# Kernel optimization log

Hardware: AMD Instinct MI355X
Metric: run time of the kernel (lower is better)

The kernel has to match this reference:

```python
import jax, jax.numpy as jnp
import numpy as np

S, B, H = 2048, 1, 1024
N_HEADS = 16
HEAD_DIM = H // N_HEADS
E, K, F = 8, 2, 2048  # experts, top_k, ffn_hidden
EPS = 1e-5


def layernorm(x, w, b):
    mu = jnp.mean(x, axis=-1, keepdims=True)
    var = jnp.mean(jnp.square(x - mu), axis=-1, keepdims=True)
    return (x - mu) * jax.lax.rsqrt(var + EPS) * w + b


def setup_inputs() -> dict:
    key = jax.random.key(0)
    ks = jax.random.split(key, 8)
    std = 0.02
    return {
        "x": jax.random.normal(ks[0], (S, B, H), dtype=jnp.float32),
        "ln1_w": jnp.ones((H,), jnp.float32),
        "ln1_b": jnp.zeros((H,), jnp.float32),
        "in_proj_w": jax.random.normal(ks[1], (3 * H, H), jnp.float32) * std,
        "in_proj_b": jnp.zeros((3 * H,), jnp.float32),
        "out_proj_w": jax.random.normal(ks[2], (H, H), jnp.float32) * std,
        "out_proj_b": jnp.zeros((H,), jnp.float32),
        "ln2_w": jnp.ones((H,), jnp.float32),
        "ln2_b": jnp.zeros((H,), jnp.float32),
        "router_w": jax.random.normal(ks[3], (E, H), jnp.float32) * std,
        "w1": jax.random.normal(ks[4], (E, H, F), jnp.float32) * std,
        "w2": jax.random.normal(ks[5], (E, F, H), jnp.float32) * std,
    }


def reference(x, ln1_w, ln1_b, in_proj_w, in_proj_b, out_proj_w, out_proj_b,
              ln2_w, ln2_b, router_w, w1, w2):
    s, b, h = x.shape
    # ---- causal self-attention (nn.MultiheadAttention math) ----
    hn = layernorm(x, ln1_w, ln1_b)
    qkv = hn @ in_proj_w.T + in_proj_b          # [S,B,3H]
    q, k, v = jnp.split(qkv, 3, axis=-1)
    q = q.reshape(s, b, N_HEADS, HEAD_DIM)
    k = k.reshape(s, b, N_HEADS, HEAD_DIM)
    v = v.reshape(s, b, N_HEADS, HEAD_DIM)
    scores = jnp.einsum('sbnd,tbnd->bnst', q, k) / np.sqrt(HEAD_DIM)
    causal = jnp.tril(jnp.ones((s, s), bool))
    scores = jnp.where(causal[None, None], scores, -jnp.inf)
    probs = jax.nn.softmax(scores, axis=-1)
    attn = jnp.einsum('bnst,tbnd->sbnd', probs, v).reshape(s, b, h)
    attn = attn @ out_proj_w.T + out_proj_b
    x1 = x + attn
    # ---- dMoE FFN: router softmax -> top-k gates -> expert GELU MLP ----
    hn2 = layernorm(x1, ln2_w, ln2_b).reshape(s * b, h)   # tokens [T,H]
    logits = hn2 @ router_w.T                              # [T,E]
    rp = jax.nn.softmax(logits, axis=-1)
    topw, topi = jax.lax.top_k(rp, K)                      # [T,K]
    gates = jnp.sum(jax.nn.one_hot(topi, E, dtype=hn2.dtype) * topw[..., None], axis=1)  # [T,E]
    hmid = jax.nn.gelu(jnp.einsum('th,ehf->tef', hn2, w1), approximate=False)  # [T,E,F]
    y = jnp.einsum('tef,efh->th', hmid * gates[:, :, None], w2)                # [T,H]
    return x1 + y.reshape(s, b, h)
```

## Files before the change

### kernel.cpp

```cpp
#include <hip/hip_runtime.h>

#define SL 2048
#define HID 1024
#define NHEAD 16
#define HD 64
#define NEXP 8
#define FF 2048
#define MAXTILE 40
#define MAXROWS (MAXTILE * 128)
#define CPAD 32

typedef short bf16x8 __attribute__((ext_vector_type(8)));
typedef float f32x4 __attribute__((ext_vector_type(4)));
typedef unsigned u32x4 __attribute__((ext_vector_type(4)));

__device__ __forceinline__ unsigned short f2bf(float f) {
  unsigned u = __builtin_bit_cast(unsigned, f);
  u += 0x7fffu + ((u >> 16) & 1u);
  return (unsigned short)(u >> 16);
}

__device__ __forceinline__ void gload16(const void* g, void* l) {
  __builtin_amdgcn_global_load_lds((const __attribute__((address_space(1))) void*)g,
                                   (__attribute__((address_space(3))) void*)l,
                                   16, 0, 0);
}

__device__ __forceinline__ void xcd_remap(int& bx, int& by) {
  const int nx = gridDim.x;
  const int nwg = nx * gridDim.y;
  const int L = by * nx + bx;
  const int per = nwg >> 3;
  const int Lp = (L & 7) * per + (L >> 3);
  bx = Lp % nx;
  by = Lp / nx;
}

struct TransLds { float Afp[64 * 128]; unsigned Bu[128 * 33]; };

__device__ __forceinline__ void trans_tile(
    int tile, const float* __restrict__ w1, const float* __restrict__ w2,
    unsigned short* __restrict__ w1t, unsigned short* __restrict__ w2t,
    int tid, TransLds* T)
{
  const int m = tile >> 8;
  const int t = tile & 255;
  const float* in;
  unsigned short* out;
  int R, C, r0, c0;
  if (m < 8) {
    in = w1 + (size_t)m * HID * FF;  out = w1t + (size_t)m * HID * FF;
    R = HID; C = FF;  r0 = (t >> 4) * 64;  c0 = (t & 15) * 128;
  } else {
    in = w2 + (size_t)(m - 8) * FF * HID;  out = w2t + (size_t)(m - 8) * FF * HID;
    R = FF; C = HID;  r0 = (t >> 3) * 64;  c0 = (t & 7) * 128;
  }
  const int wv = tid >> 6, ln = tid & 63;
#pragma unroll
  for (int p = 0; p < 8; p++) {
    const int ebase = p * 1024 + wv * 256;
    const int eo = ebase + ln * 4;
    const int r = eo >> 7, c = eo & 127;
    gload16(in + (size_t)(r0 + r) * C + c0 + c, (char*)T->Afp + (size_t)ebase * 4);
  }
  asm volatile("s_waitcnt vmcnt(0)" ::: "memory");
  __syncthreads();
#pragma unroll
  for (int it = 0; it < 16; it++) {
    const int idx = it * 256 + tid;
    const int rp = idx >> 7;
    const int c = idx & 127;
    const float v0 = T->Afp[(2 * rp) * 128 + c];
    const float v1 = T->Afp[(2 * rp + 1) * 128 + c];
    T->Bu[c * 33 + rp] = (unsigned)f2bf(v0) | ((unsigned)f2bf(v1) << 16);
  }
  __syncthreads();
#pragma unroll
  for (int it = 0; it < 8; it++) {
    const int idx = it * 256 + tid;
    const int c = idx >> 4;
    const int r4 = (idx & 15) * 4;
    const unsigned u0 = T->Bu[c * 33 + (r4 >> 1)];
    const unsigned u1 = T->Bu[c * 33 + (r4 >> 1) + 1];
    ushort4 u;
    u.x = (unsigned short)(u0 & 0xffff);
    u.y = (unsigned short)(u0 >> 16);
    u.z = (unsigned short)(u1 & 0xffff);
    u.w = (unsigned short)(u1 >> 16);
    *reinterpret_cast<ushort4*>(&out[(size_t)(c0 + c) * R + r0 + r4]) = u;
  }
}

#define PIPE_WAIT(i, NT)                                                     \
  if ((i) == (NT) - 1)                                                       \
    asm volatile("s_waitcnt vmcnt(0) lgkmcnt(0)" ::: "memory");              \
  else                                                                       \
    asm volatile("s_waitcnt vmcnt(4) lgkmcnt(0)" ::: "memory");              \
  __builtin_amdgcn_s_barrier();

#define GEMM_FRAGS_MFMA(CC)                                                  \
  bf16x8 af[4], bfr[4];                                                      \
  _Pragma("unroll")                                                          \
  for (int mt = 0; mt < 4; mt++)                                             \
    af[mt] = *reinterpret_cast<const bf16x8*>(                               \
        &Asm[CC][(wm + mt * 16 + la) * 32 + lk]);                            \
  _Pragma("unroll")                                                          \
  for (int nt = 0; nt < 4; nt++)                                             \
    bfr[nt] = *reinterpret_cast<const bf16x8*>(                              \
        &Bsm[CC][(wn + nt * 16 + la) * 32 + lk]);                            \
  __builtin_amdgcn_s_setprio(1);                                             \
  _Pragma("unroll")                                                          \
  for (int mt = 0; mt < 4; mt++)                                             \
    _Pragma("unroll")                                                        \
    for (int nt = 0; nt < 4; nt++)                                           \
      acc[mt][nt] =                                                          \
          __builtin_amdgcn_mfma_f32_16x16x32_bf16(af[mt], bfr[nt], acc[mt][nt], 0, 0, 0); \
  __builtin_amdgcn_s_setprio(0);

#define PIPE_ROT()                                                           \
  cc = (cc == 2) ? 0 : cc + 1;                                               \
  cs = (cs == 2) ? 0 : cs + 1;

__global__ __launch_bounds__(256) void qkv_trans_kernel(
    const unsigned short* __restrict__ A, const unsigned short* __restrict__ Bt,
    const float* __restrict__ bias,
    unsigned short* __restrict__ q_out, unsigned short* __restrict__ k_out,
    unsigned short* __restrict__ vt_out,
    const float* __restrict__ w1, const float* __restrict__ w2,
    unsigned short* __restrict__ w1t, unsigned short* __restrict__ w2t)
{
  __shared__ union {
    struct { unsigned short A[3][4096]; unsigned short B[3][4096]; } g;
    TransLds t;
  } sm;
  const int tid = threadIdx.x;

  if (blockIdx.z == 0) {
    unsigned short (*Asm)[4096] = sm.g.A;
    unsigned short (*Bsm)[4096] = sm.g.B;
    int bx = blockIdx.x, by = blockIdx.y;
    xcd_remap(bx, by);
    const int wave = tid >> 6;
    const int lane = tid & 63;
    const int m0 = by * 128;
    const int n0 = bx * 128;
    const int wm = (wave >> 1) * 64;
    const int wn = (wave & 1) * 64;
    const int la = lane & 15;
    const int lk = (lane >> 4) * 8;

    f32x4 acc[4][4] = {};

    const int srow = tid >> 2;
    const int skoff = (tid & 3) * 8;
    const unsigned short* Ag = A + (size_t)(m0 + srow) * HID + skoff;
    const unsigned short* Bg = Bt + (size_t)(n0 + srow) * HID + skoff;

    auto stage = [&](int s, int k0) {
      gload16(Ag + k0, &Asm[s][wave * 512]);
      gload16(Ag + (size_t)64 * HID + k0, &Asm[s][2048 + wave * 512]);
      gload16(Bg + k0, &Bsm[s][wave * 512]);
      gload16(Bg + (size_t)64 * HID + k0, &Bsm[s][2048 + wave * 512]);
    };

    stage(0, 0);
    stage(1, 32);
    const int NT = HID >> 5;
    int cc = 0, cs = 2;
    for (int i = 0; i < NT; ++i) {
      PIPE_WAIT(i, NT)
      if (i + 2 < NT) stage(cs, (i + 2) << 5);
      GEMM_FRAGS_MFMA(cc)
      PIPE_ROT()
    }

    const int lg = lane >> 4;
#pragma unroll
    for (int mt = 0; mt < 4; mt++) {
#pragma unroll
      for (int nt = 0; nt < 4; nt++) {
#pragma unroll
        for (int r = 0; r < 4; r++) {
          const int row = m0 + wm + mt * 16 + lg * 4 + r;
          const int col = n0 + wn + nt * 16 + la;
          float v = acc[mt][nt][r] + bias[col];
          const int hh = (col & 1023) >> 6;
          const int dd = col & 63;
          const unsigned short bv = f2bf(v);
          if (col < 1024)
            q_out[(size_t)hh * SL * HD + (size_t)row * HD + dd] = bv;
          else if (col < 2048)
            k_out[(size_t)hh * SL * HD + (size_t)row * HD + dd] = bv;
          else
            vt_out[(size_t)hh * HD * SL + (size_t)dd * SL + row] = bv;
        }
      }
    }
  } else {
    const int id = blockIdx.y * 24 + blockIdx.x;
    const int tile = 512 + ((int)blockIdx.z - 1) * 384 + id;
    trans_tile(tile, w1, w2, w1t, w2t, tid, &sm.t);
  }
}

__global__ __launch_bounds__(256) void gemm_bt2(
    const unsigned short* __restrict__ A, const unsigned short* __restrict__ Bt,
    float* __restrict__ outf,
    const float* __restrict__ w1, const float* __restrict__ w2,
    unsigned short* __restrict__ w1t, unsigned short* __restrict__ w2t)
{
  __shared__ union {
    struct { unsigned short A[3][4096]; unsigned short B[3][4096]; } g;
    TransLds t;
  } sm;
  const int tid = threadIdx.x;

  if (blockIdx.z >= 2) {
    const int id = blockIdx.y * 8 + blockIdx.x;
    const int tile = 3200 + ((int)blockIdx.z - 2) * 128 + id;
    trans_tile(tile, w1, w2, w1t, w2t, tid, &sm.t);
    return;
  }

  unsigned short (*Asm)[4096] = sm.g.A;
  unsigned short (*Bsm)[4096] = sm.g.B;
  int bx = blockIdx.x, by = blockIdx.y;
  xcd_remap(bx, by);
  const int wave = tid >> 6;
  const int lane = tid & 63;
  const int m0 = by * 128;
  const int n0 = bx * 128;
  const int koff = blockIdx.z * (HID / 2);
  const int wm = (wave >> 1) * 64;
  const int wn = (wave & 1) * 64;
  const int la = lane & 15;
  const int lk = (lane >> 4) * 8;

  f32x4 acc[4][4] = {};

  const int srow = tid >> 2;
  const int skoff = (tid & 3) * 8;
  const unsigned short* Ag = A + (size_t)(m0 + srow) * HID + koff + skoff;
  const unsigned short* Bg = Bt + (size_t)(n0 + srow) * HID + koff + skoff;

  auto stage = [&](int s, int k0) {
    gload16(Ag + k0, &Asm[s][wave * 512]);
    gload16(Ag + (size_t)64 * HID + k0, &Asm[s][2048 + wave * 512]);
    gload16(Bg + k0, &Bsm[s][wave * 512]);
    gload16(Bg + (size_t)64 * HID + k0, &Bsm[s][2048 + wave * 512]);
  };

  stage(0, 0);
  stage(1, 32);
  const int NT = (HID / 2) >> 5;
  int cc = 0, cs = 2;
  for (int i = 0; i < NT; ++i) {
    PIPE_WAIT(i, NT)
    if (i + 2 < NT) stage(cs, (i + 2) << 5);
    GEMM_FRAGS_MFMA(cc)
    PIPE_ROT()
  }

  const int lg = lane >> 4;
#pragma unroll
  for (int mt = 0; mt < 4; mt++) {
#pragma unroll
    for (int nt = 0; nt < 4; nt++) {
#pragma unroll
      for (int r = 0; r < 4; r++) {
        const int row = m0 + wm + mt * 16 + lg * 4 + r;
        const int col = n0 + wn + nt * 16 + la;
        outf[(size_t)blockIdx.z * SL * HID + (size_t)row * HID + col] = acc[mt][nt][r];
      }
    }
  }
}

__global__ __launch_bounds__(256) void gemm_moe1(
    const unsigned short* __restrict__ A, const unsigned short* __restrict__ w1t,
    const int* __restrict__ perm, const float* __restrict__ gateg,
    const int* __restrict__ texp, const int* __restrict__ trow,
    unsigned short* __restrict__ hmidg)
{
  __shared__ unsigned short Asm[3][128 * 32];
  __shared__ unsigned short Bsm[3][128 * 32];
  int bx = blockIdx.x, by = blockIdx.y;
  xcd_remap(bx, by);
  const int e = texp[by];
  if (e < 0) return;
  const int row0 = trow[by];
  const int tid = threadIdx.x;
  const int wave = tid >> 6;
  const int lane = tid & 63;
  const int n0 = bx * 128;
  const int wm = (wave >> 1) * 64;
  const int wn = (wave & 1) * 64;
  const int la = lane & 15;
  const int lk = (lane >> 4) * 8;
  f32x4 acc[4][4] = {};

  const int srow = tid >> 2;
  const int skoff = (tid & 3) * 8;
  const int p0 = perm[row0 + srow];
  const int p1 = perm[row0 + 64 + srow];
  const unsigned short* Ag0 = A + (size_t)(p0 < 0 ? 0 : (p0 >> 1)) * HID + skoff;
  const unsigned short* Ag1 = A + (size_t)(p1 < 0 ? 0 : (p1 >> 1)) * HID + skoff;
  const unsigned short* Bg = w1t + (size_t)e * HID * FF + (size_t)(n0 + srow) * HID + skoff;

  auto stage = [&](int s, int k0) {
    gload16(Ag0 + k0, &Asm[s][wave * 512]);
    gload16(Ag1 + k0, &Asm[s][2048 + wave * 512]);
    gload16(Bg + k0, &Bsm[s][wave * 512]);
    gload16(Bg + (size_t)64 * HID + k0, &Bsm[s][2048 + wave * 512]);
  };

  stage(0, 0);
  stage(1, 32);
  const int NT = HID >> 5;
  int cc = 0, cs = 2;
  for (int i = 0; i < NT; ++i) {
    PIPE_WAIT(i, NT)
    if (i + 2 < NT) stage(cs, (i + 2) << 5);
    GEMM_FRAGS_MFMA(cc)
    PIPE_ROT()
  }

  const int lg = lane >> 4;
#pragma unroll
  for (int mt = 0; mt < 4; mt++) {
    float gr[4];
#pragma unroll
    for (int r = 0; r < 4; r++) gr[r] = gateg[row0 + wm + mt * 16 + lg * 4 + r];
#pragma unroll
    for (int nt = 0; nt < 4; nt++) {
#pragma unroll
      for (int r = 0; r < 4; r++) {
        const int grow = row0 + wm + mt * 16 + lg * 4 + r;
        const int col = n0 + wn + nt * 16 + la;
        const float v = acc[mt][nt][r];
        const float g = 0.5f * v * (1.0f + erff(v * 0.70710678118f));
        hmidg[(size_t)grow * FF + col] = f2bf(g * gr[r]);
      }
    }
  }
}

__global__ __launch_bounds__(256) void gemm_moe2(
    const unsigned short* __restrict__ A, const unsigned short* __restrict__ w2t,
    const int* __restrict__ perm,
    const int* __restrict__ texp, const int* __restrict__ trow,
    float* __restrict__ ybuf)
{
  __shared__ unsigned short Asm[3][128 * 32];
  __shared__ unsigned short Bsm[3][128 * 32];
  int bx = blockIdx.x, by = blockIdx.y;
  xcd_remap(bx, by);
  const int e = texp[by];
  if (e < 0) return;
  const int row0 = trow[by];
  const int tid = threadIdx.x;
  const int wave = tid >> 6;
  const int lane = tid & 63;
  const int n0 = bx * 128;
  const int koff = blockIdx.z * (FF / 2);
  const int wm = (wave >> 1) * 64;
  const int wn = (wave & 1) * 64;
  const int la = lane & 15;
  const int lk = (lane >> 4) * 8;
  f32x4 acc[4][4] = {};

  const int srow = tid >> 2;
  const int skoff = (tid & 3) * 8;
  const unsigned short* Ag = A + (size_t)(row0 + srow) * FF + koff + skoff;
  const unsigned short* Bg = w2t + (size_t)e * FF * HID + (size_t)(n0 + srow) * FF + koff + skoff;

  auto stage = [&](int s, int k0) {
    gload16(Ag + k0, &Asm[s][wave * 512]);
    gload16(Ag + (size_t)64 * FF + k0, &Asm[s][2048 + wave * 512]);
    gload16(Bg + k0, &Bsm[s][wave * 512]);
    gload16(Bg + (size_t)64 * FF + k0, &Bsm[s][2048 + wave * 512]);
  };

  stage(0, 0);
  stage(1, 32);
  const int NT = (FF / 2) >> 5;
  int cc = 0, cs = 2;
  for (int i = 0; i < NT; ++i) {
    PIPE_WAIT(i, NT)
    if (i + 2 < NT) stage(cs, (i + 2) << 5);
    GEMM_FRAGS_MFMA(cc)
    PIPE_ROT()
  }

  const int lg = lane >> 4;
#pragma unroll
  for (int mt = 0; mt < 4; mt++) {
    int pr[4];
#pragma unroll
    for (int r = 0; r < 4; r++) pr[r] = perm[row0 + wm + mt * 16 + lg * 4 + r];
#pragma unroll
    for (int nt = 0; nt < 4; nt++) {
#pragma unroll
      for (int r = 0; r < 4; r++) {
        const int p = pr[r];
        if (p >= 0) {
          const int col = n0 + wn + nt * 16 + la;
          ybuf[(size_t)(blockIdx.z * 2 + (p & 1)) * SL * HID + (size_t)(p >> 1) * HID + col] =
              acc[mt][nt][r];
        }
      }
    }
  }
}

__global__ __launch_bounds__(256) void ln_conv_kernel(
    const float* __restrict__ x, const float* __restrict__ w, const float* __restrict__ b,
    unsigned short* __restrict__ ob,
    const float4* __restrict__ cva, const float4* __restrict__ cvb,
    ushort4* __restrict__ coa, ushort4* __restrict__ cob,
    const float* __restrict__ w1, const float* __restrict__ w2,
    unsigned short* __restrict__ w1t, unsigned short* __restrict__ w2t)
{
  __shared__ union { struct { float ps[4], pq[4]; } l; TransLds t; } sm;
  const int tid = threadIdx.x;
  if ((int)blockIdx.x < SL) {
    const int row = blockIdx.x;
    const float4 v = *reinterpret_cast<const float4*>(&x[(size_t)row * HID + tid * 4]);
    float s = v.x + v.y + v.z + v.w;
    float q = v.x * v.x + v.y * v.y + v.z * v.z + v.w * v.w;
    for (int off = 32; off > 0; off >>= 1) {
      s += __shfl_down(s, off);
      q += __shfl_down(q, off);
    }
    const int wave = tid >> 6, lane = tid & 63;
    if (lane == 0) { sm.l.ps[wave] = s; sm.l.pq[wave] = q; }
    __syncthreads();
    s = sm.l.ps[0] + sm.l.ps[1] + sm.l.ps[2] + sm.l.ps[3];
    q = sm.l.pq[0] + sm.l.pq[1] + sm.l.pq[2] + sm.l.pq[3];
    const float mu = s * (1.0f / HID);
    const float inv = rsqrtf(q * (1.0f / HID) - mu * mu + 1e-5f);
    const int i = tid * 4;
    const float4 wv = *reinterpret_cast<const float4*>(&w[i]);
    const float4 bv = *reinterpret_cast<const float4*>(&b[i]);
    ushort4 u;
    u.x = f2bf((v.x - mu) * inv * wv.x + bv.x);
    u.y = f2bf((v.y - mu) * inv * wv.y + bv.y);
    u.z = f2bf((v.z - mu) * inv * wv.z + bv.z);
    u.w = f2bf((v.w - mu) * inv * wv.w + bv.w);
    *reinterpret_cast<ushort4*>(&ob[(size_t)row * HID + i]) = u;
  } else if ((int)blockIdx.x < SL + 512) {
    const int NA = 3 * HID * HID / 4, NB = HID * HID / 4;
    for (int i = ((int)blockIdx.x - SL) * 256 + tid; i < NA + NB; i += 512 * 256) {
      if (i < NA) {
        const float4 v = cva[i];
        ushort4 u; u.x = f2bf(v.x); u.y = f2bf(v.y); u.z = f2bf(v.z); u.w = f2bf(v.w);
        coa[i] = u;
      } else {
        const float4 v = cvb[i - NA];
        ushort4 u; u.x = f2bf(v.x); u.y = f2bf(v.y); u.z = f2bf(v.z); u.w = f2bf(v.w);
        cob[i - NA] = u;
      }
    }
  } else {
    const int tile = (int)blockIdx.x - SL - 512;
    trans_tile(tile, w1, w2, w1t, w2t, tid, &sm.t);
  }
}

__global__ __launch_bounds__(256) void combine_ln(
    const float4* __restrict__ x, const float* __restrict__ bias,
    const float4* __restrict__ p0, const float4* __restrict__ p1,
    float4* __restrict__ x1,
    const float* __restrict__ w, const float* __restrict__ b,
    unsigned short* __restrict__ ob, float* __restrict__ of)
{
  const int row = blockIdx.x;
  const int tid = threadIdx.x;
  const int i4 = row * 256 + tid;
  const int i = tid * 4;
  const float4 bv0 = *reinterpret_cast<const float4*>(&bias[i]);
  const float4 a = x[i4], c = p0[i4], d = p1[i4];
  float4 v;
  v.x = a.x + bv0.x + c.x + d.x;
  v.y = a.y + bv0.y + c.y + d.y;
  v.z = a.z + bv0.z + c.z + d.z;
  v.w = a.w + bv0.w + c.w + d.w;
  x1[i4] = v;
  float s = v.x + v.y + v.z + v.w;
  float q = v.x * v.x + v.y * v.y + v.z * v.z + v.w * v.w;
  for (int off = 32; off > 0; off >>= 1) {
    s += __shfl_down(s, off);
    q += __shfl_down(q, off);
  }
  __shared__ float ps[4], pq[4];
  const int wave = tid >> 6, lane = tid & 63;
  if (lane == 0) { ps[wave] = s; pq[wave] = q; }
  __syncthreads();
  s = ps[0] + ps[1] + ps[2] + ps[3];
  q = pq[0] + pq[1] + pq[2] + pq[3];
  const float mu = s * (1.0f / HID);
  const float inv = rsqrtf(q * (1.0f / HID) - mu * mu + 1e-5f);
  const float4 wv = *reinterpret_cast<const float4*>(&w[i]);
  const float4 bv = *reinterpret_cast<const float4*>(&b[i]);
  const float o0 = (v.x - mu) * inv * wv.x + bv.x;
  const float o1 = (v.y - mu) * inv * wv.y + bv.y;
  const float o2 = (v.z - mu) * inv * wv.z + bv.z;
  const float o3 = (v.w - mu) * inv * wv.w + bv.w;
  ushort4 u; u.x = f2bf(o0); u.y = f2bf(o1); u.z = f2bf(o2); u.w = f2bf(o3);
  *reinterpret_cast<ushort4*>(&ob[(size_t)row * HID + i]) = u;
  float4 o; o.x = o0; o.y = o1; o.z = o2; o.w = o3;
  *reinterpret_cast<float4*>(&of[(size_t)row * HID + i]) = o;
}

__global__ __launch_bounds__(256) void router_kernel(
    const float* __restrict__ hn2f, const float* __restrict__ rw,
    int* __restrict__ ti, float* __restrict__ tg, int* __restrict__ cnt)
{
  __shared__ float wlds[NEXP * HID];
  __shared__ int lcnt[NEXP];
  const int tid = threadIdx.x;
#pragma unroll
  for (int i = 0; i < 8; i++)
    *reinterpret_cast<float4*>(&wlds[i * 1024 + tid * 4]) =
        *reinterpret_cast<const float4*>(&rw[i * 1024 + tid * 4]);
  if (tid < NEXP) lcnt[tid] = 0;
  __syncthreads();

  const int wave = tid >> 6, lane = tid & 63;
#pragma unroll 1
  for (int k = 0; k < 4; k++) {
    const int t = blockIdx.x * 16 + wave * 4 + k;
    float4 xr[4];
#pragma unroll
    for (int c = 0; c < 4; c++)
      xr[c] = *reinterpret_cast<const float4*>(&hn2f[(size_t)t * HID + c * 256 + lane * 4]);
    float p[NEXP];
#pragma unroll
    for (int e = 0; e < NEXP; e++) {
      float s = 0.f;
#pragma unroll
      for (int c = 0; c < 4; c++) {
        const float4 wv = *reinterpret_cast<const float4*>(&wlds[e * 1024 + c * 256 + lane * 4]);
        s += xr[c].x * wv.x + xr[c].y * wv.y + xr[c].z * wv.z + xr[c].w * wv.w;
      }
      s += __shfl_xor(s, 32);
      s += __shfl_xor(s, 16);
      s += __shfl_xor(s, 8);
      s += __shfl_xor(s, 4);
      s += __shfl_xor(s, 2);
      s += __shfl_xor(s, 1);
      p[e] = s;
    }
    if (lane == 0) {
      float mx = p[0];
#pragma unroll
      for (int e = 1; e < NEXP; e++) mx = fmaxf(mx, p[e]);
      float Z = 0.f;
#pragma unroll
      for (int e = 0; e < NEXP; e++) { p[e] = expf(p[e] - mx); Z += p[e]; }
      const float invZ = 1.f / Z;
      int i1 = 0;
#pragma unroll
      for (int e = 1; e < NEXP; e++) if (p[e] > p[i1]) i1 = e;
      int i2 = (i1 == 0) ? 1 : 0;
#pragma unroll
      for (int e = 0; e < NEXP; e++) if (e != i1 && p[e] > p[i2]) i2 = e;
      ti[2 * t] = i1; ti[2 * t + 1] = i2;
      tg[2 * t] = p[i1] * invZ; tg[2 * t + 1] = p[i2] * invZ;
      atomicAdd(&lcnt[i1], 1);
      atomicAdd(&lcnt[i2], 1);
    }
  }
  __syncthreads();
  if (tid < NEXP && lcnt[tid] > 0) atomicAdd(&cnt[tid * CPAD], lcnt[tid]);
}

__global__ void scan_kernel(const int* __restrict__ cnt, int* __restrict__ poff,
                            int* __restrict__ texp, int* __restrict__ trow)
{
  if (threadIdx.x == 0 && blockIdx.x == 0) {
    int off = 0, nt = 0;
    for (int e = 0; e < NEXP; e++) {
      poff[e] = off;
      const int c = cnt[e * CPAD];
      const int ntl = (c + 127) >> 7;
      for (int i = 0; i < ntl; i++) { texp[nt] = e; trow[nt] = off + i * 128; nt++; }
      off += ntl * 128;
    }
    for (int i = nt; i < MAXTILE; i++) { texp[i] = -1; trow[i] = 0; }
  }
}

__global__ __launch_bounds__(256) void build_kernel(
    const int* __restrict__ ti, const float* __restrict__ tg,
    const int* __restrict__ poff, int* __restrict__ fill,
    int* __restrict__ perm, float* __restrict__ gateg)
{
  __shared__ int lcnt[NEXP], lbase[NEXP];
  const int tid = threadIdx.x;
  if (tid < NEXP) lcnt[tid] = 0;
  __syncthreads();
  const int t = blockIdx.x * 256 + tid;
  int e0 = ti[2 * t], e1 = ti[2 * t + 1];
  int l0 = atomicAdd(&lcnt[e0], 1);
  int l1 = atomicAdd(&lcnt[e1], 1);
  __syncthreads();
  if (tid < NEXP) lbase[tid] = (lcnt[tid] > 0) ? atomicAdd(&fill[tid * CPAD], lcnt[tid]) : 0;
  __syncthreads();
  int pos0 = poff[e0] + lbase[e0] + l0;
  int pos1 = poff[e1] + lbase[e1] + l1;
  perm[pos0] = 2 * t;
  gateg[pos0] = tg[2 * t];
  perm[pos1] = 2 * t + 1;
  gateg[pos1] = tg[2 * t + 1];
}

__global__ __launch_bounds__(256) void final_add(
    const float4* __restrict__ x1, const float4* __restrict__ y0,
    const float4* __restrict__ y1, const float4* __restrict__ y2,
    const float4* __restrict__ y3, float4* __restrict__ out)
{
  const int i = blockIdx.x * 256 + threadIdx.x;
  const float4 a = x1[i], b = y0[i], c = y1[i], d = y2[i], e = y3[i];
  float4 o;
  o.x = a.x + b.x + c.x + d.x + e.x;
  o.y = a.y + b.y + c.y + d.y + e.y;
  o.z = a.z + b.z + c.z + d.z + e.z;
  o.w = a.w + b.w + c.w + d.w + e.w;
  out[i] = o;
}

#define SC2 0.1803368801111204f
#define PPITCH 20
__global__ __launch_bounds__(512) void attn_kernel(
    const unsigned short* __restrict__ qb, const unsigned short* __restrict__ kb,
    const unsigned short* __restrict__ vtb, unsigned short* __restrict__ attn)
{
  const int h = blockIdx.y;
  const int tid = threadIdx.x;
  const int wave = tid >> 6, lane = tid & 63;
  const int grp = wave >> 2;
  const int w4 = wave & 3;
  const int la = lane & 15, lg = lane >> 4;
  const int la7 = la & 7;
  __shared__ unsigned short Kt[2][2][64 * 64];
  __shared__ unsigned short Vt[2][2][64 * 64];
  __shared__ unsigned plds[8 * 32 * PPITCH];
  const unsigned short* qh = qb + (size_t)h * SL * HD;
  const unsigned short* kh = kb + (size_t)h * SL * HD;
  const unsigned short* vh = vtb + (size_t)h * HD * SL;
  unsigned* pu = &plds[wave * 32 * PPITCH];

  const int sr_lo = w4 * 8 + (lane >> 3);
  const int ss = lane & 7;

  auto stageKV = [&](int t, int buf) {
    const int kvb = t * 64;
#pragma unroll
    for (int j = 0; j < 2; j++) {
      const int row = j * 32 + sr_lo;
      const int s = ss ^ (row & 7);
      gload16(kh + (size_t)(kvb + row) * HD + s * 8, &Kt[grp][buf][j * 2048 + w4 * 512]);
      gload16(vh + (size_t)row * SL + kvb + s * 8, &Vt[grp][buf][j * 2048 + w4 * 512]);
    }
  };

  for (int half = 0; half < 2; half++) {
    const int qt = half ? (31 - blockIdx.x) : blockIdx.x;
    const int m0 = qt * 64 + w4 * 16;
    const int T = qt + 1;
    const int S = (T + 1) >> 1;
    const int q = m0 + la;

    bf16x8 aq0 = *reinterpret_cast<const bf16x8*>(&qh[(size_t)(m0 + la) * HD + lg * 8]);
    bf16x8 aq1 = *reinterpret_cast<const bf16x8*>(&qh[(size_t)(m0 + la) * HD + 32 + lg * 8]);

    f32x4 oacc[4] = {};
    float mrun = -1e30f, lrun = 0.f;

    if (grp < T) stageKV(grp, 0);
    __syncthreads();
    int cur = 0;

    for (int s = 0; s < S; s++) {
      const int tmy = 2 * s + grp;
      if (tmy + 2 < T) stageKV(tmy + 2, cur ^ 1);
      if (tmy < T) {
        const int kv0 = tmy * 64;
        const unsigned short* Kb = Kt[grp][cur];
        const unsigned short* Vb = Vt[grp][cur];

        f32x4 sac[4] = {};
        __builtin_amdgcn_s_setprio(1);
#pragma unroll
        for (int nt = 0; nt < 4; nt++) {
          const int row = nt * 16 + la;
          bf16x8 b0 = *reinterpret_cast<const bf16x8*>(&Kb[row * 64 + ((lg ^ la7) << 3)]);
          bf16x8 b1 = *reinterpret_cast<const bf16x8*>(&Kb[row * 64 + (((4 + lg) ^ la7) << 3)]);
          sac[nt] = __builtin_amdgcn_mfma_f32_16x16x32_bf16(b0, aq0, sac[nt], 0, 0, 0);
          sac[nt] = __builtin_amdgcn_mfma_f32_16x16x32_bf16(b1, aq1, sac[nt], 0, 0, 0);
        }
        __builtin_amdgcn_s_setprio(0);
        float sv[4][4];
        const bool diag = (tmy == qt);
#pragma unroll
        for (int nt = 0; nt < 4; nt++)
#pragma unroll
          for (int r = 0; r < 4; r++) {
            float xs = sac[nt][r] * SC2;
            if (diag && (kv0 + nt * 16 + lg * 4 + r) > q) xs = -1e30f;
            sv[nt][r] = xs;
          }
        float pm = fmaxf(fmaxf(sv[0][0], sv[0][1]), fmaxf(sv[0][2], sv[0][3]));
#pragma unroll
        for (int nt = 1; nt < 4; nt++)
          pm = fmaxf(pm, fmaxf(fmaxf(sv[nt][0], sv[nt][1]), fmaxf(sv[nt][2], sv[nt][3])));
        pm = fmaxf(pm, __shfl_xor(pm, 16));
        pm = fmaxf(pm, __shfl_xor(pm, 32));
        const float mn = fmaxf(mrun, pm);
        float rs = 0.f;
#pragma unroll
        for (int nt = 0; nt < 4; nt++)
#pragma unroll
          for (int r = 0; r < 4; r++) {
            const float pe = exp2f(sv[nt][r] - mn);
            sv[nt][r] = pe;
            rs += pe;
          }
        rs += __shfl_xor(rs, 16);
        rs += __shfl_xor(rs, 32);
        if (__ballot(pm > mrun) != 0ULL) {
          const float al = exp2f(mrun - mn);
#pragma unroll
          for (int dt = 0; dt < 4; dt++)
#pragma unroll
            for (int r = 0; r < 4; r++) oacc[dt][r] *= al;
          lrun = lrun * al + rs;
          mrun = mn;
        } else {
          lrun += rs;
        }
#pragma unroll
        for (int nt = 0; nt < 4; nt++)
#pragma unroll
          for (int rp = 0; rp < 2; rp++) {
            unsigned pk;
            asm("v_cvt_pk_bf16_f32 %0, %1, %2"
                : "=v"(pk) : "v"(sv[nt][rp * 2]), "v"(sv[nt][rp * 2 + 1]));
            pu[(nt * 8 + lg * 2 + rp) * PPITCH + la] = pk;
          }
        asm volatile("s_waitcnt lgkmcnt(0)" ::: "memory");
        __builtin_amdgcn_sched_barrier(0);
        u32x4 w0, w1;
#pragma unroll
        for (int jj = 0; jj < 4; jj++) {
          w0[jj] = pu[(lg * 4 + jj) * PPITCH + la];
          w1[jj] = pu[(16 + lg * 4 + jj) * PPITCH + la];
        }
        const bf16x8 pa0 = __builtin_bit_cast(bf16x8, w0);
        const bf16x8 pa1 = __builtin_bit_cast(bf16x8, w1);
        __builtin_amdgcn_s_setprio(1);
#pragma unroll
        for (int dt = 0; dt < 4; dt++) {
          const int row = dt * 16 + la;
          bf16x8 v0 = *reinterpret_cast<const bf16x8*>(&Vb[row * 64 + ((lg ^ la7) << 3)]);
          bf16x8 v1 = *reinterpret_cast<const bf16x8*>(&Vb[row * 64 + (((4 + lg) ^ la7) << 3)]);
          oacc[dt] = __builtin_amdgcn_mfma_f32_16x16x32_bf16(v0, pa0, oacc[dt], 0, 0, 0);
          oacc[dt] = __builtin_amdgcn_mfma_f32_16x16x32_bf16(v1, pa1, oacc[dt], 0, 0, 0);
        }
        __builtin_amdgcn_s_setprio(0);
      }
      __syncthreads();
      cur ^= 1;
    }

    float* xb = (float*)&Kt[0][0][0];
    float* mlb = (float*)&Vt[0][0][0];
    if (grp == 1) {
#pragma unroll
      for (int dt = 0; dt < 4; dt++)
#pragma unroll
        for (int r = 0; r < 4; r++)
          xb[w4 * 1024 + (dt * 16 + lg * 4 + r) * 16 + la] = oacc[dt][r];
      if (lg == 0) {
        mlb[w4 * 32 + la * 2] = mrun;
        mlb[w4 * 32 + la * 2 + 1] = lrun;
      }
    }
    __syncthreads();
    if (grp == 0) {
      const float m1 = mlb[w4 * 32 + la * 2];
      const float l1 = mlb[w4 * 32 + la * 2 + 1];
      const float mm = fmaxf(mrun, m1);
      const float a0 = exp2f(mrun - mm);
      const float a1 = exp2f(m1 - mm);
      const float linv = 1.0f / (lrun * a0 + l1 * a1);
#pragma unroll
      for (int dt = 0; dt < 4; dt++) {
        ushort4 u;
        float o0 = (oacc[dt][0] * a0 + xb[w4 * 1024 + (dt * 16 + lg * 4 + 0) * 16 + la] * a1) * linv;
        float o1 = (oacc[dt][1] * a0 + xb[w4 * 1024 + (dt * 16 + lg * 4 + 1) * 16 + la] * a1) * linv;
        float o2 = (oacc[dt][2] * a0 + xb[w4 * 1024 + (dt * 16 + lg * 4 + 2) * 16 + la] * a1) * linv;
        float o3 = (oacc[dt][3] * a0 + xb[w4 * 1024 + (dt * 16 + lg * 4 + 3) * 16 + la] * a1) * linv;
        u.x = f2bf(o0); u.y = f2bf(o1); u.z = f2bf(o2); u.w = f2bf(o3);
        *reinterpret_cast<ushort4*>(&attn[(size_t)q * HID + h * HD + dt * 16 + lg * 4]) = u;
      }
    }
    __syncthreads();
  }
}

extern "C" void kernel_launch(void* const* d_in, const int* in_sizes, int n_in,
                              void* d_out, int out_size, void* d_ws, size_t ws_size,
                              hipStream_t stream)
{
  const float* x          = (const float*)d_in[0];
  const float* ln1_w      = (const float*)d_in[1];
  const float* ln1_b      = (const float*)d_in[2];
  const float* in_proj_w  = (const float*)d_in[3];
  const float* in_proj_b  = (const float*)d_in[4];
  const float* out_proj_w = (const float*)d_in[5];
  const float* out_proj_b = (const float*)d_in[6];
  const float* ln2_w      = (const float*)d_in[7];
  const float* ln2_b      = (const float*)d_in[8];
  const float* router_w   = (const float*)d_in[9];
  const float* w1         = (const float*)d_in[10];
  const float* w2         = (const float*)d_in[11];
  float* out = (float*)d_out;

  char* ws = (char*)d_ws;
  size_t off = 0;
  auto alloc = [&](size_t bytes) -> void* {
    void* p = ws + off;
    off += (bytes + 255) & ~(size_t)255;
    return p;
  };
  unsigned short* hn_b   = (unsigned short*)alloc((size_t)SL * HID * 2);
  unsigned short* ipw_b  = (unsigned short*)alloc((size_t)3 * HID * HID * 2);
  unsigned short* opw_b  = (unsigned short*)alloc((size_t)HID * HID * 2);
  unsigned short* qb     = (unsigned short*)alloc((size_t)SL * HID * 2);
  unsigned short* kb     = (unsigned short*)alloc((size_t)SL * HID * 2);
  unsigned short* vtb    = (unsigned short*)alloc((size_t)SL * HID * 2);
  unsigned short* attn_b = (unsigned short*)alloc((size_t)SL * HID * 2);
  float*          x1     = (float*)alloc((size_t)SL * HID * 4);
  float*          pbuf   = (float*)alloc((size_t)2 * SL * HID * 4);
  unsigned short* hn2_b  = (unsigned short*)alloc((size_t)SL * HID * 2);
  float*          hn2_f  = (float*)alloc((size_t)SL * HID * 4);
  unsigned short* w1t    = (unsigned short*)alloc((size_t)NEXP * HID * FF * 2);
  unsigned short* w2t    = (unsigned short*)alloc((size_t)NEXP * HID * FF * 2);
  unsigned short* hmidg  = (unsigned short*)alloc((size_t)MAXROWS * FF * 2);
  float*          ybuf   = (float*)alloc((size_t)4 * SL * HID * 4);
  int*            ti     = (int*)alloc((size_t)SL * 2 * 4);
  float*          tg     = (float*)alloc((size_t)SL * 2 * 4);
  int*            perm   = (int*)alloc((size_t)MAXROWS * 4);
  float*          gateg  = (float*)alloc((size_t)MAXROWS * 4);
  int*            cnt    = (int*)alloc(NEXP * CPAD * 4);
  int*            fill   = (int*)alloc(NEXP * CPAD * 4);
  int*            poff   = (int*)alloc(64 * 4);
  int*            texp   = (int*)alloc(64 * 4);
  int*            trow   = (int*)alloc(64 * 4);

  const dim3 blk(256);

  hipMemsetAsync(cnt, 0, NEXP * CPAD * 4, stream);
  hipMemsetAsync(fill, 0, NEXP * CPAD * 4, stream);
  hipMemsetAsync(perm, 0xFF, (size_t)MAXROWS * 4, stream);
  hipMemsetAsync(gateg, 0, (size_t)MAXROWS * 4, stream);

  ln_conv_kernel<<<SL + 1024, blk, 0, stream>>>(
      x, ln1_w, ln1_b, hn_b,
      (const float4*)in_proj_w, (const float4*)out_proj_w,
      (ushort4*)ipw_b, (ushort4*)opw_b,
      w1, w2, w1t, w2t);

  qkv_trans_kernel<<<dim3(3 * HID / 128, SL / 128, 8), blk, 0, stream>>>(
      hn_b, ipw_b, in_proj_b, qb, kb, vtb, w1, w2, w1t, w2t);

  attn_kernel<<<dim3(16, NHEAD), dim3(512), 0, stream>>>(qb, kb, vtb, attn_b);

  gemm_bt2<<<dim3(HID / 128, SL / 128, 9), blk, 0, stream>>>(
      attn_b, opw_b, pbuf, w1, w2, w1t, w2t);

  combine_ln<<<SL, blk, 0, stream>>>(
      (const float4*)x, out_proj_b, (const float4*)pbuf,
      (const float4*)(pbuf + (size_t)SL * HID), (float4*)x1,
      ln2_w, ln2_b, hn2_b, hn2_f);

  router_kernel<<<SL / 16, blk, 0, stream>>>(hn2_f, router_w, ti, tg, cnt);
  scan_kernel<<<1, 64, 0, stream>>>(cnt, poff, texp, trow);
  build_kernel<<<SL / 256, blk, 0, stream>>>(ti, tg, poff, fill, perm, gateg);

  gemm_moe1<<<dim3(FF / 128, MAXTILE), blk, 0, stream>>>(
      hn2_b, w1t, perm, gateg, texp, trow, hmidg);
  gemm_moe2<<<dim3(HID / 128, MAXTILE, 2), blk, 0, stream>>>(
      hmidg, w2t, perm, texp, trow, ybuf);

  final_add<<<SL * HID / 1024, blk, 0, stream>>>(
      (const float4*)x1, (const float4*)ybuf,
      (const float4*)(ybuf + (size_t)SL * HID),
      (const float4*)(ybuf + (size_t)2 * SL * HID),
      (const float4*)(ybuf + (size_t)3 * SL * HID),
      (float4*)out);
}
```

Before: 250.3 us.

## Fuse router into combine_ln and merge scan/build into one kernel

Computes router logits, softmax and top-2 selection inside the combine+layernorm kernel, so the fp32 hn2 buffer is no longer written and reread. Scan and permutation build are merged into a single one-block kernel, which removes two launches and the fill memset. The trade-off is that the build step is now serialized in one block with shared atomics, and every row does global atomics on cnt. Permutation order within an expert is nondeterministic, though each token still gets its correct gate.

```diff
diff --git a/kernel.cpp b/kernel.cpp
--- a/kernel.cpp
+++ b/kernel.cpp
@@ -472,8 +472,12 @@
     const float4* __restrict__ p0, const float4* __restrict__ p1,
     float4* __restrict__ x1,
     const float* __restrict__ w, const float* __restrict__ b,
-    unsigned short* __restrict__ ob, float* __restrict__ of)
-{
+    unsigned short* __restrict__ ob,
+    const float* __restrict__ rw,
+    int* __restrict__ ti, float* __restrict__ tg, int* __restrict__ cnt)
+{
+  __shared__ float ps[4], pq[4];
+  __shared__ float rsm[4][8];
   const int row = blockIdx.x;
   const int tid = threadIdx.x;
   const int i4 = row * 256 + tid;
@@ -492,7 +496,6 @@
     s += __shfl_down(s, off);
     q += __shfl_down(q, off);
   }
-  __shared__ float ps[4], pq[4];
   const int wave = tid >> 6, lane = tid & 63;
   if (lane == 0) { ps[wave] = s; pq[wave] = q; }
   __syncthreads();
@@ -508,77 +511,62 @@
   const float o3 = (v.w - mu) * inv * wv.w + bv.w;
   ushort4 u; u.x = f2bf(o0); u.y = f2bf(o1); u.z = f2bf(o2); u.w = f2bf(o3);
   *reinterpret_cast<ushort4*>(&ob[(size_t)row * HID + i]) = u;
-  float4 o; o.x = o0; o.y = o1; o.z = o2; o.w = o3;
-  *reinterpret_cast<float4*>(&of[(size_t)row * HID + i]) = o;
-}
-
-__global__ __launch_bounds__(256) void router_kernel(
-    const float* __restrict__ hn2f, const float* __restrict__ rw,
-    int* __restrict__ ti, float* __restrict__ tg, int* __restrict__ cnt)
-{
-  __shared__ float wlds[NEXP * HID];
-  __shared__ int lcnt[NEXP];
+
+  float pl[NEXP];
+#pragma unroll
+  for (int e = 0; e < NEXP; e++) {
+    const float4 rv = *reinterpret_cast<const float4*>(&rw[e * HID + i]);
+    pl[e] = o0 * rv.x + o1 * rv.y + o2 * rv.z + o3 * rv.w;
+  }
+#pragma unroll
+  for (int e = 0; e < NEXP; e++) {
+    pl[e] += __shfl_xor(pl[e], 32);
+    pl[e] += __shfl_xor(pl[e], 16);
+    pl[e] += __shfl_xor(pl[e], 8);
+    pl[e] += __shfl_xor(pl[e], 4);
+    pl[e] += __shfl_xor(pl[e], 2);
+    pl[e] += __shfl_xor(pl[e], 1);
+  }
+  if (lane == 0) {
+#pragma unroll
+    for (int e = 0; e < NEXP; e++) rsm[wave][e] = pl[e];
+  }
+  __syncthreads();
+  if (tid == 0) {
+    float lgt[NEXP];
+#pragma unroll
+    for (int e = 0; e < NEXP; e++)
+      lgt[e] = rsm[0][e] + rsm[1][e] + rsm[2][e] + rsm[3][e];
+    float mx = lgt[0];
+#pragma unroll
+    for (int e = 1; e < NEXP; e++) mx = fmaxf(mx, lgt[e]);
+    float Z = 0.f;
+    float pexp[NEXP];
+#pragma unroll
+    for (int e = 0; e < NEXP; e++) { pexp[e] = expf(lgt[e] - mx); Z += pexp[e]; }
+    const float invZ = 1.f / Z;
+    int i1 = 0;
+#pragma unroll
+    for (int e = 1; e < NEXP; e++) if (pexp[e] > pexp[i1]) i1 = e;
+    int i2 = (i1 == 0) ? 1 : 0;
+#pragma unroll
+    for (int e = 0; e < NEXP; e++) if (e != i1 && pexp[e] > pexp[i2]) i2 = e;
+    ti[2 * row] = i1; ti[2 * row + 1] = i2;
+    tg[2 * row] = pexp[i1] * invZ; tg[2 * row + 1] = pexp[i2] * invZ;
+    atomicAdd(&cnt[i1 * CPAD], 1);
+    atomicAdd(&cnt[i2 * CPAD], 1);
+  }
+}
+
+__global__ __launch_bounds__(256) void scan_build_kernel(
+    const int* __restrict__ cnt, const int* __restrict__ ti, const float* __restrict__ tg,
+    int* __restrict__ texp, int* __restrict__ trow,
+    int* __restrict__ perm, float* __restrict__ gateg)
+{
+  __shared__ int poff[NEXP];
+  __shared__ int lfill[NEXP];
   const int tid = threadIdx.x;
-#pragma unroll
-  for (int i = 0; i < 8; i++)
-    *reinterpret_cast<float4*>(&wlds[i * 1024 + tid * 4]) =
-        *reinterpret_cast<const float4*>(&rw[i * 1024 + tid * 4]);
-  if (tid < NEXP) lcnt[tid] = 0;
-  __syncthreads();
-
-  const int wave = tid >> 6, lane = tid & 63;
-#pragma unroll 1
-  for (int k = 0; k < 4; k++) {
-    const int t = blockIdx.x * 16 + wave * 4 + k;
-    float4 xr[4];
-#pragma unroll
-    for (int c = 0; c < 4; c++)
-      xr[c] = *reinterpret_cast<const float4*>(&hn2f[(size_t)t * HID + c * 256 + lane * 4]);
-    float p[NEXP];
-#pragma unroll
-    for (int e = 0; e < NEXP; e++) {
-      float s = 0.f;
-#pragma unroll
-      for (int c = 0; c < 4; c++) {
-        const float4 wv = *reinterpret_cast<const float4*>(&wlds[e * 1024 + c * 256 + lane * 4]);
-        s += xr[c].x * wv.x + xr[c].y * wv.y + xr[c].z * wv.z + xr[c].w * wv.w;
-      }
-      s += __shfl_xor(s, 32);
-      s += __shfl_xor(s, 16);
-      s += __shfl_xor(s, 8);
-      s += __shfl_xor(s, 4);
-      s += __shfl_xor(s, 2);
-      s += __shfl_xor(s, 1);
-      p[e] = s;
-    }
-    if (lane == 0) {
-      float mx = p[0];
-#pragma unroll
-      for (int e = 1; e < NEXP; e++) mx = fmaxf(mx, p[e]);
-      float Z = 0.f;
-#pragma unroll
-      for (int e = 0; e < NEXP; e++) { p[e] = expf(p[e] - mx); Z += p[e]; }
-      const float invZ = 1.f / Z;
-      int i1 = 0;
-#pragma unroll
-      for (int e = 1; e < NEXP; e++) if (p[e] > p[i1]) i1 = e;
-      int i2 = (i1 == 0) ? 1 : 0;
-#pragma unroll
-      for (int e = 0; e < NEXP; e++) if (e != i1 && p[e] > p[i2]) i2 = e;
-      ti[2 * t] = i1; ti[2 * t + 1] = i2;
-      tg[2 * t] = p[i1] * invZ; tg[2 * t + 1] = p[i2] * invZ;
-      atomicAdd(&lcnt[i1], 1);
-      atomicAdd(&lcnt[i2], 1);
-    }
-  }
-  __syncthreads();
-  if (tid < NEXP && lcnt[tid] > 0) atomicAdd(&cnt[tid * CPAD], lcnt[tid]);
-}
-
-__global__ void scan_kernel(const int* __restrict__ cnt, int* __restrict__ poff,
-                            int* __restrict__ texp, int* __restrict__ trow)
-{
-  if (threadIdx.x == 0 && blockIdx.x == 0) {
+  if (tid == 0) {
     int off = 0, nt = 0;
     for (int e = 0; e < NEXP; e++) {
       poff[e] = off;
@@ -589,30 +577,18 @@
     }
     for (int i = nt; i < MAXTILE; i++) { texp[i] = -1; trow[i] = 0; }
   }
-}
-
-__global__ __launch_bounds__(256) void build_kernel(
-    const int* __restrict__ ti, const float* __restrict__ tg,
-    const int* __restrict__ poff, int* __restrict__ fill,
-    int* __restrict__ perm, float* __restrict__ gateg)
-{
-  __shared__ int lcnt[NEXP], lbase[NEXP];
-  const int tid = threadIdx.x;
-  if (tid < NEXP) lcnt[tid] = 0;
+  if (tid < NEXP) lfill[tid] = 0;
   __syncthreads();
-  const int t = blockIdx.x * 256 + tid;
-  int e0 = ti[2 * t], e1 = ti[2 * t + 1];
-  int l0 = atomicAdd(&lcnt[e0], 1);
-  int l1 = atomicAdd(&lcnt[e1], 1);
-  __syncthreads();
-  if (tid < NEXP) lbase[tid] = (lcnt[tid] > 0) ? atomicAdd(&fill[tid * CPAD], lcnt[tid]) : 0;
-  __syncthreads();
-  int pos0 = poff[e0] + lbase[e0] + l0;
-  int pos1 = poff[e1] + lbase[e1] + l1;
-  perm[pos0] = 2 * t;
-  gateg[pos0] = tg[2 * t];
-  perm[pos1] = 2 * t + 1;
-  gateg[pos1] = tg[2 * t + 1];
+  for (int t = tid; t < SL; t += 256) {
+#pragma unroll
+    for (int s2 = 0; s2 < 2; s2++) {
+      const int e = ti[2 * t + s2];
+      const int l = atomicAdd(&lfill[e], 1);
+      const int pos = poff[e] + l;
+      perm[pos] = 2 * t + s2;
+      gateg[pos] = tg[2 * t + s2];
+    }
+  }
 }
 
 __global__ __launch_bounds__(256) void final_add(
@@ -845,7 +821,6 @@
   float*          x1     = (float*)alloc((size_t)SL * HID * 4);
   float*          pbuf   = (float*)alloc((size_t)2 * SL * HID * 4);
   unsigned short* hn2_b  = (unsigned short*)alloc((size_t)SL * HID * 2);
-  float*          hn2_f  = (float*)alloc((size_t)SL * HID * 4);
   unsigned short* w1t    = (unsigned short*)alloc((size_t)NEXP * HID * FF * 2);
   unsigned short* w2t    = (unsigned short*)alloc((size_t)NEXP * HID * FF * 2);
   unsigned short* hmidg  = (unsigned short*)alloc((size_t)MAXROWS * FF * 2);
@@ -855,15 +830,14 @@
   int*            perm   = (int*)alloc((size_t)MAXROWS * 4);
   float*          gateg  = (float*)alloc((size_t)MAXROWS * 4);
   int*            cnt    = (int*)alloc(NEXP * CPAD * 4);
-  int*            fill   = (int*)alloc(NEXP * CPAD * 4);
   int*            poff   = (int*)alloc(64 * 4);
   int*            texp   = (int*)alloc(64 * 4);
   int*            trow   = (int*)alloc(64 * 4);
+  (void)poff;
 
   const dim3 blk(256);
 
   hipMemsetAsync(cnt, 0, NEXP * CPAD * 4, stream);
-  hipMemsetAsync(fill, 0, NEXP * CPAD * 4, stream);
   hipMemsetAsync(perm, 0xFF, (size_t)MAXROWS * 4, stream);
   hipMemsetAsync(gateg, 0, (size_t)MAXROWS * 4, stream);
 
@@ -884,11 +858,10 @@
   combine_ln<<<SL, blk, 0, stream>>>(
       (const float4*)x, out_proj_b, (const float4*)pbuf,
       (const float4*)(pbuf + (size_t)SL * HID), (float4*)x1,
-      ln2_w, ln2_b, hn2_b, hn2_f);
-
-  router_kernel<<<SL / 16, blk, 0, stream>>>(hn2_f, router_w, ti, tg, cnt);
-  scan_kernel<<<1, 64, 0, stream>>>(cnt, poff, texp, trow);
-  build_kernel<<<SL / 256, blk, 0, stream>>>(ti, tg, poff, fill, perm, gateg);
+      ln2_w, ln2_b, hn2_b,
+      router_w, ti, tg, cnt);
+
+  scan_build_kernel<<<1, blk, 0, stream>>>(cnt, ti, tg, texp, trow, perm, gateg);
 
   gemm_moe1<<<dim3(FF / 128, MAXTILE), blk, 0, stream>>>(
       hn2_b, w1t, perm, gateg, texp, trow, hmidg);
```

Result: faster. 244.8 us, median of 2 (-2.2%).
